# Optimization experiments

Hardware: AMD Instinct MI355X
Metric: run time of the kernel (lower is better)

## Reference

```python
import jax, jax.numpy as jnp
import numpy as np

N_HEADS = 8
N_FILTERS = 512
HEAD_DIM = N_FILTERS // N_HEADS  # key_dim == value_dim == 64
BATCH = 32
SEQ = 4096


def setup_inputs() -> dict:
    key = jax.random.key(0)
    ks = jax.random.split(key, 9)
    s_in = 1.0 / np.sqrt(N_FILTERS)
    s_out = 1.0 / np.sqrt(N_HEADS * HEAD_DIM)
    return {
        "x": jax.random.normal(ks[0], (BATCH, SEQ, N_FILTERS), dtype=jnp.float32),
        # stacked per-head projection weights, stored as [H, in, out]
        "Wq": jax.random.uniform(ks[1], (N_HEADS, N_FILTERS, HEAD_DIM), jnp.float32, -s_in, s_in),
        "bq": jax.random.uniform(ks[2], (N_HEADS, HEAD_DIM), jnp.float32, -s_in, s_in),
        "Wk": jax.random.uniform(ks[3], (N_HEADS, N_FILTERS, HEAD_DIM), jnp.float32, -s_in, s_in),
        "bk": jax.random.uniform(ks[4], (N_HEADS, HEAD_DIM), jnp.float32, -s_in, s_in),
        "Wv": jax.random.uniform(ks[5], (N_HEADS, N_FILTERS, HEAD_DIM), jnp.float32, -s_in, s_in),
        "bv": jax.random.uniform(ks[6], (N_HEADS, HEAD_DIM), jnp.float32, -s_in, s_in),
        "Wo": jax.random.uniform(ks[7], (N_HEADS * HEAD_DIM, N_FILTERS), jnp.float32, -s_out, s_out),
        "bo": jax.random.uniform(ks[8], (N_FILTERS,), jnp.float32, -s_out, s_out),
    }


def reference(x, Wq, bq, Wk, bk, Wv, bv, Wo, bo):
    B, L, F = x.shape
    # Per-head projections, batched over heads: [H, B, L, D]
    Q = jnp.einsum("blf,hfd->hbld", x, Wq) + bq[:, None, None, :]
    K = jnp.einsum("blf,hfd->hbld", x, Wk) + bk[:, None, None, :]
    V = jnp.einsum("blf,hfd->hbld", x, Wv) + bv[:, None, None, :]
    # Feature-space attention: Q^T K -> [H, B, D, D], scale, softmax over dim=1 (rows)
    scores = jnp.einsum("hbld,hble->hbde", Q, K) / np.sqrt(HEAD_DIM).astype(np.float32)
    A = jax.nn.softmax(scores, axis=-2)
    # heads[i] = V @ A : [H, B, L, D]
    heads = jnp.einsum("hbld,hbde->hble", V, A)
    # Faithful to torch: heads.view(batch, l, -1) reinterprets the [H,B,L,D] buffer
    out = heads.reshape(B, L, N_HEADS * HEAD_DIM)
    return out @ Wo + bo
```

## Files before the change

### kernel.cpp

```cpp
#include <hip/hip_runtime.h>
#include <hip/hip_bf16.h>
#include <cstdint>
#include <cstddef>

#define BATCH 32
#define SEQ   4096
#define NF    512
#define NH    8
#define HD    64

typedef __bf16 bf16x8 __attribute__((ext_vector_type(8)));
typedef float  f32x4  __attribute__((ext_vector_type(4)));

__device__ __forceinline__ int lds_off(int m, int kg) {
  return (((m >> 4) * 4 + kg) * 16 + (m & 15)) * 8;
}

template<int MODE>
struct SRegs { bf16x8 h0, h1, l0, l1; };

__device__ __forceinline__ void cvt8(const float* f, bf16x8& vh, bf16x8& vl) {
#pragma unroll
  for (int j = 0; j < 8; ++j) {
    float x = f[j];
    __bf16 h = (__bf16)x;
    vh[j] = h;
    vl[j] = (__bf16)(x - (float)h);
  }
}

template<int MODE>
__device__ __forceinline__ SRegs<MODE> stage_load(
    const void* pa, const void* pb, long long zoff, int ld,
    long long row0, int k0, int tid)
{
  SRegs<MODE> R;
  if constexpr (MODE == 0 || MODE == 3) {
    const __bf16* hi = (const __bf16*)pa + zoff;
    const int r = tid >> 1, half = tid & 1;
    const size_t base = (size_t)(row0 + r) * ld + k0 + half * 16;
    R.h0 = *(const bf16x8*)(hi + base);
    R.h1 = *(const bf16x8*)(hi + base + 8);
    if constexpr (MODE == 0) {
      const __bf16* lo = (const __bf16*)pb + zoff;
      R.l0 = *(const bf16x8*)(lo + base);
      R.l1 = *(const bf16x8*)(lo + base + 8);
    }
  } else if constexpr (MODE == 1) {
    const float* A = (const float*)pa + zoff;
    const int r = tid >> 1, half = tid & 1;
    const float* src = A + (size_t)(row0 + r) * ld + k0 + half * 16;
    float f[16];
#pragma unroll
    for (int q = 0; q < 4; ++q) {
      float4 v = *(const float4*)&src[q * 4];
      f[q * 4 + 0] = v.x; f[q * 4 + 1] = v.y; f[q * 4 + 2] = v.z; f[q * 4 + 3] = v.w;
    }
    cvt8(f, R.h0, R.l0);
    cvt8(f + 8, R.h1, R.l1);
  } else {
    const float* A = (const float*)pa + zoff;
    const int m = tid & 127, lg = (tid >> 7) * 16;
    float f[16];
#pragma unroll
    for (int i = 0; i < 16; ++i)
      f[i] = A[(size_t)(k0 + lg + i) * ld + row0 + m];
    cvt8(f, R.h0, R.l0);
    cvt8(f + 8, R.h1, R.l1);
  }
  return R;
}

template<int MODE>
__device__ __forceinline__ void stage_store(
    const SRegs<MODE>& R, __bf16* sH, __bf16* sL, int tid)
{
  if constexpr (MODE == 2) {
    const int m = tid & 127, kq = (tid >> 7) * 2;
    *(bf16x8*)&sH[lds_off(m, kq + 0)] = R.h0;
    *(bf16x8*)&sH[lds_off(m, kq + 1)] = R.h1;
    *(bf16x8*)&sL[lds_off(m, kq + 0)] = R.l0;
    *(bf16x8*)&sL[lds_off(m, kq + 1)] = R.l1;
  } else {
    const int r = tid >> 1, kq = (tid & 1) * 2;
    *(bf16x8*)&sH[lds_off(r, kq + 0)] = R.h0;
    *(bf16x8*)&sH[lds_off(r, kq + 1)] = R.h1;
    if constexpr (MODE != 3) {
      *(bf16x8*)&sL[lds_off(r, kq + 0)] = R.l0;
      *(bf16x8*)&sL[lds_off(r, kq + 1)] = R.l1;
    }
  }
}

template<int MA, int MB, int EPI>
__global__ __launch_bounds__(256) void mfma_nt(
    const void* Aa, const void* Ab, long long sA, int lda,
    const void* Ba, const void* Bb, long long sB, int ldb,
    const float* __restrict__ bias, void* C0, void* C1, long long sC, int K)
{
  constexpr bool AL = (MA != 3);
  __shared__ __bf16 smem[(AL ? 4 : 3) * 4096];
  __bf16* sAh = smem;
  __bf16* sBh = smem + 4096;
  __bf16* sBl = smem + 8192;
  __bf16* sAl = AL ? (smem + 12288) : smem;

  const int tid = threadIdx.x;
  const int lane = tid & 63, wave = tid >> 6;
  const int wm = wave >> 1, wn = wave & 1;

  const unsigned nx = gridDim.x, ny = gridDim.y;
  const unsigned nwg = nx * ny * gridDim.z;
  unsigned bid = blockIdx.x + nx * (blockIdx.y + ny * blockIdx.z);
  unsigned nid = (bid & 7) * (nwg >> 3) + (bid >> 3);
  const unsigned bx = nid % nx;
  unsigned t = nid / nx;
  const unsigned by = t % ny;
  const unsigned z = t / ny;

  const long long m0 = (long long)by * 128;
  const int n0 = bx * 128;
  const long long zA = (long long)z * sA, zB = (long long)z * sB;

  f32x4 acc[4][4];
#pragma unroll
  for (int i = 0; i < 4; ++i)
#pragma unroll
    for (int j = 0; j < 4; ++j)
#pragma unroll
      for (int c = 0; c < 4; ++c) acc[i][j][c] = 0.f;

  const int kg = lane >> 4, r = lane & 15;

  SRegs<MA> ra = stage_load<MA>(Aa, Ab, zA, lda, m0, 0, tid);
  SRegs<MB> rb = stage_load<MB>(Ba, Bb, zB, ldb, n0, 0, tid);

  for (int k0 = 0; k0 < K; k0 += 32) {
    __syncthreads();
    stage_store<MA>(ra, sAh, sAl, tid);
    stage_store<MB>(rb, sBh, sBl, tid);
    __syncthreads();
    if (k0 + 32 < K) {
      ra = stage_load<MA>(Aa, Ab, zA, lda, m0, k0 + 32, tid);
      rb = stage_load<MB>(Ba, Bb, zB, ldb, n0, k0 + 32, tid);
    }

    bf16x8 ah[4], al[4], bh[4], bl[4];
#pragma unroll
    for (int i = 0; i < 4; ++i) {
      ah[i] = *(const bf16x8*)&sAh[lds_off(wm * 64 + i * 16 + r, kg)];
      if constexpr (AL)
        al[i] = *(const bf16x8*)&sAl[lds_off(wm * 64 + i * 16 + r, kg)];
      bh[i] = *(const bf16x8*)&sBh[lds_off(wn * 64 + i * 16 + r, kg)];
      bl[i] = *(const bf16x8*)&sBl[lds_off(wn * 64 + i * 16 + r, kg)];
    }
#pragma unroll
    for (int i = 0; i < 4; ++i)
#pragma unroll
      for (int j = 0; j < 4; ++j) {
        acc[i][j] = __builtin_amdgcn_mfma_f32_16x16x32_bf16(ah[i], bh[j], acc[i][j], 0, 0, 0);
        if constexpr (AL)
          acc[i][j] = __builtin_amdgcn_mfma_f32_16x16x32_bf16(al[i], bh[j], acc[i][j], 0, 0, 0);
        acc[i][j] = __builtin_amdgcn_mfma_f32_16x16x32_bf16(ah[i], bl[j], acc[i][j], 0, 0, 0);
      }
  }

  const int rbase = (lane >> 4) * 4;
  const int cn = lane & 15;
#pragma unroll
  for (int i = 0; i < 4; ++i) {
    const long long gm = m0 + wm * 64 + i * 16 + rbase;
#pragma unroll
    for (int j = 0; j < 4; ++j) {
      const int gn = n0 + wn * 64 + j * 16 + cn;
      if constexpr (EPI == 0) {
        float* C = (float*)C0 + (long long)z * sC;
#pragma unroll
        for (int rr = 0; rr < 4; ++rr)
          C[(size_t)(gm + rr) * 512 + gn] = acc[i][j][rr];
      } else if constexpr (EPI == 1) {
        float* C = (float*)C0;
        const float bv = bias[gn];
#pragma unroll
        for (int rr = 0; rr < 4; ++rr)
          C[(size_t)(gm + rr) * 512 + gn] = acc[i][j][rr] + bv;
      } else if constexpr (EPI == 2) {
        __bf16* Ch = (__bf16*)C0 + (long long)z * sC;
        __bf16* Cl = (__bf16*)C1 + (long long)z * sC;
#pragma unroll
        for (int rr = 0; rr < 4; ++rr) {
          float v = acc[i][j][rr];
          __bf16 h = (__bf16)v;
          Ch[(size_t)(gm + rr) * 512 + gn] = h;
          Cl[(size_t)(gm + rr) * 512 + gn] = (__bf16)(v - (float)h);
        }
      } else {
        const int h = gn >> 6, e = gn & 63;
        const float bv = bias[(h * 32 + (int)z) * 64 + e];
        __bf16* Ch = (__bf16*)C0;
        const size_t rowb = (size_t)(h * 32 + (int)z) * 4096 + gm;
#pragma unroll
        for (int rr = 0; rr < 4; ++rr)
          Ch[(rowb + rr) * 64 + e] = (__bf16)(acc[i][j][rr] + bv);
      }
    }
  }
}

__global__ void pack3_kernel(const float* __restrict__ Wq, const float* __restrict__ Wk,
                             const float* __restrict__ Wv, const float* __restrict__ Wo,
                             float* __restrict__ Wq_all, float* __restrict__ Wk_all,
                             float* __restrict__ Wv_all,
                             __bf16* __restrict__ Wkt_h, __bf16* __restrict__ Wkt_l,
                             __bf16* __restrict__ Wot_h, __bf16* __restrict__ Wot_l) {
  int i = blockIdx.x * 256 + threadIdx.x;
  if (i >= NF * NF) return;
  int f = i >> 9, n = i & 511, h = n >> 6, d = n & 63;
  size_t src = ((size_t)h * NF + f) * HD + d;
  float wq = Wq[src], wk = Wk[src], wv = Wv[src];
  Wq_all[i] = wq;
  Wk_all[i] = wk;
  Wv_all[i] = wv;
  __bf16 kh = (__bf16)wk;
  Wkt_h[(size_t)n * 512 + f] = kh;
  Wkt_l[(size_t)n * 512 + f] = (__bf16)(wk - (float)kh);
  float wo = Wo[i];
  __bf16 oh = (__bf16)wo;
  Wot_h[(size_t)n * 512 + f] = oh;
  Wot_l[(size_t)n * 512 + f] = (__bf16)(wo - (float)oh);
}

__global__ __launch_bounds__(256) void colsum_kernel(const float* __restrict__ x,
                                                     float* __restrict__ s_part) {
  const int b = blockIdx.x, c = blockIdx.y, t = threadIdx.x;
  const float* base = x + ((size_t)b * SEQ + c * 256) * NF;
  float a0 = 0.f, a1 = 0.f;
  for (int l = 0; l < 256; ++l) {
    a0 += base[(size_t)l * NF + t];
    a1 += base[(size_t)l * NF + t + 256];
  }
  float* o = s_part + ((size_t)b * 16 + c) * NF;
  o[t] = a0;
  o[t + 256] = a1;
}

__global__ __launch_bounds__(256) void pqk_kernel(
    const float* __restrict__ s_part, const float* __restrict__ Wq_all,
    const float* __restrict__ Wk_all, float* __restrict__ pq, float* __restrict__ pk) {
  const int b = blockIdx.x, t = threadIdx.x;
  __shared__ float s[512];
  float a0 = 0.f, a1 = 0.f;
  for (int c = 0; c < 16; ++c) {
    a0 += s_part[((size_t)b * 16 + c) * NF + t];
    a1 += s_part[((size_t)b * 16 + c) * NF + t + 256];
  }
  s[t] = a0;
  s[t + 256] = a1;
  __syncthreads();
  float q0 = 0.f, q1 = 0.f, k0 = 0.f, k1 = 0.f;
  for (int f = 0; f < NF; ++f) {
    const float sv = s[f];
    q0 += sv * Wq_all[(size_t)f * NF + t];
    q1 += sv * Wq_all[(size_t)f * NF + t + 256];
    k0 += sv * Wk_all[(size_t)f * NF + t];
    k1 += sv * Wk_all[(size_t)f * NF + t + 256];
  }
  pq[(size_t)b * NF + t] = q0;
  pq[(size_t)b * NF + t + 256] = q1;
  pk[(size_t)b * NF + t] = k0;
  pk[(size_t)b * NF + t + 256] = k1;
}

__global__ __launch_bounds__(256) void score_softmax_kernel(
    const float* __restrict__ Wq_all, const float* __restrict__ U,
    const float* __restrict__ pq, const float* __restrict__ pk,
    const float* __restrict__ bq, const float* __restrict__ bk,
    const float* __restrict__ bv,
    float* __restrict__ Amat, float* __restrict__ bvA) {
  const int hb = blockIdx.x;
  const int h = hb >> 5, b = hb & 31;
  __shared__ float Qs[64][65];
  __shared__ float Us[64][65];
  __shared__ float Ss[64][65];
  const int tid = threadIdx.x, eg = tid & 15, dg = tid >> 4;
  const float* Ub = U + (size_t)b * NF * NF;

  float acc[4][4];
#pragma unroll
  for (int i = 0; i < 4; ++i)
#pragma unroll
    for (int j = 0; j < 4; ++j) acc[i][j] = 0.f;

  for (int f0 = 0; f0 < NF; f0 += 64) {
#pragma unroll
    for (int q = 0; q < 4; ++q) {
      const int idx = q * 256 + tid;
      const int fi = idx >> 4, dd = (idx & 15) * 4;
      *(float4*)&Qs[fi][dd] = *(const float4*)&Wq_all[(size_t)(f0 + fi) * NF + h * HD + dd];
      *(float4*)&Us[fi][dd] = *(const float4*)&Ub[(size_t)(f0 + fi) * NF + h * HD + dd];
    }
    __syncthreads();
#pragma unroll 16
    for (int fi = 0; fi < 64; ++fi) {
      float4 qa = *(float4*)&Qs[fi][dg * 4];
      float4 ub = *(float4*)&Us[fi][eg * 4];
      float qa_[4] = {qa.x, qa.y, qa.z, qa.w};
      float ub_[4] = {ub.x, ub.y, ub.z, ub.w};
#pragma unroll
      for (int i = 0; i < 4; ++i)
#pragma unroll
        for (int j = 0; j < 4; ++j) acc[i][j] = fmaf(qa_[i], ub_[j], acc[i][j]);
    }
    __syncthreads();
  }

#pragma unroll
  for (int i = 0; i < 4; ++i) {
    const int d = dg * 4 + i;
    const float bqv = bq[h * HD + d];
    const float pqv = pq[(size_t)b * NF + h * HD + d];
#pragma unroll
    for (int j = 0; j < 4; ++j) {
      const int e = eg * 4 + j;
      const float bkv = bk[h * HD + e];
      const float pkv = pk[(size_t)b * NF + h * HD + e];
      float v = acc[i][j] + bqv * pkv + bkv * pqv + 4096.f * bqv * bkv;
      Ss[d][e] = v * 0.125f;
    }
  }
  __syncthreads();

  if (tid < 64) {
    const int e = tid;
    float m = -INFINITY;
    for (int d = 0; d < 64; ++d) m = fmaxf(m, Ss[d][e]);
    float sum = 0.f;
    for (int d = 0; d < 64; ++d) {
      float ex = __expf(Ss[d][e] - m);
      Ss[d][e] = ex;
      sum += ex;
    }
    const float inv = 1.f / sum;
    float bacc = 0.f;
    for (int d = 0; d < 64; ++d) {
      const float a = Ss[d][e] * inv;
      Amat[(size_t)hb * 4096 + d * 64 + e] = a;
      bacc = fmaf(bv[h * HD + d], a, bacc);
    }
    bvA[(size_t)hb * HD + e] = bacc;
  }
}

__global__ __launch_bounds__(256) void wva_kernel(
    const float* __restrict__ Wv_all, const float* __restrict__ Amat,
    __bf16* __restrict__ WvAt_h, __bf16* __restrict__ WvAt_l) {
  const int hb = blockIdx.y, h = hb >> 5, b = hb & 31;
  const int f0 = blockIdx.x * 128;
  __shared__ float Ws[128][65];
  __shared__ float As[64][65];
  const int tid = threadIdx.x;

#pragma unroll
  for (int q = 0; q < 4; ++q) {
    const int idx = q * 256 + tid;
    const int d = idx >> 4, ee = (idx & 15) * 4;
    *(float4*)&As[d][ee] = *(const float4*)&Amat[(size_t)hb * 4096 + d * 64 + ee];
  }
#pragma unroll
  for (int q = 0; q < 8; ++q) {
    const int idx = q * 256 + tid;
    const int fi = idx >> 4, dd = (idx & 15) * 4;
    *(float4*)&Ws[fi][dd] = *(const float4*)&Wv_all[(size_t)(f0 + fi) * NF + h * HD + dd];
  }
  __syncthreads();

  const int fg = tid >> 4, eg = tid & 15;
  float acc[8][4];
#pragma unroll
  for (int i = 0; i < 8; ++i)
#pragma unroll
    for (int j = 0; j < 4; ++j) acc[i][j] = 0.f;
#pragma unroll 8
  for (int d = 0; d < 64; ++d) {
    float4 av = *(float4*)&As[d][eg * 4];
    float a_[4] = {av.x, av.y, av.z, av.w};
#pragma unroll
    for (int i = 0; i < 8; ++i) {
      const float w = Ws[fg * 8 + i][d];
#pragma unroll
      for (int j = 0; j < 4; ++j) acc[i][j] = fmaf(w, a_[j], acc[i][j]);
    }
  }

  __syncthreads();
  float* Ts = &Ws[0][0];
#pragma unroll
  for (int i = 0; i < 8; ++i)
#pragma unroll
    for (int j = 0; j < 4; ++j)
      Ts[(eg * 4 + j) * 130 + fg * 8 + i] = acc[i][j];
  __syncthreads();

  const int e = tid >> 2, fs = (tid & 3) * 32;
  size_t orow = ((size_t)b * 512 + h * 64 + e) * 512 + f0 + fs;
#pragma unroll
  for (int c = 0; c < 4; ++c) {
    bf16x8 vh, vl;
#pragma unroll
    for (int j = 0; j < 8; ++j) {
      float v = Ts[e * 130 + fs + c * 8 + j];
      __bf16 hh = (__bf16)v;
      vh[j] = hh;
      vl[j] = (__bf16)(v - (float)hh);
    }
    *(bf16x8*)&WvAt_h[orow + c * 8] = vh;
    *(bf16x8*)&WvAt_l[orow + c * 8] = vl;
  }
}

extern "C" void kernel_launch(void* const* d_in, const int* in_sizes, int n_in,
                              void* d_out, int out_size, void* d_ws, size_t ws_size,
                              hipStream_t stream) {
  const float* x  = (const float*)d_in[0];
  const float* Wq = (const float*)d_in[1];
  const float* bq = (const float*)d_in[2];
  const float* Wk = (const float*)d_in[3];
  const float* bk = (const float*)d_in[4];
  const float* Wv = (const float*)d_in[5];
  const float* bv = (const float*)d_in[6];
  const float* Wo = (const float*)d_in[7];
  const float* bo = (const float*)d_in[8];
  float* out = (float*)d_out;
  (void)in_sizes; (void)n_in; (void)out_size; (void)ws_size;

  float* w = (float*)d_ws;
  size_t off = 0;
  float* Wq_all = w + off; off += 262144;
  float* Wk_all = w + off; off += 262144;
  float* Wv_all = w + off; off += 262144;
  float* s_part = w + off; off += 262144;
  float* pq     = w + off; off += 16384;
  float* pk     = w + off; off += 16384;
  float* U      = w + off; off += (size_t)32 * 262144;
  float* Amat   = w + off; off += 1048576;
  float* bvA    = w + off; off += 16384;
  __bf16* Wkt_h = (__bf16*)(w + off); off += 131072;
  __bf16* Wkt_l = (__bf16*)(w + off); off += 131072;
  __bf16* Wot_h = (__bf16*)(w + off); off += 131072;
  __bf16* Wot_l = (__bf16*)(w + off); off += 131072;
  __bf16* Gh    = (__bf16*)(w + off); off += (size_t)32 * 131072;
  __bf16* Gl    = (__bf16*)(w + off); off += (size_t)32 * 131072;
  __bf16* WvAt_h= (__bf16*)(w + off); off += (size_t)32 * 131072;
  __bf16* WvAt_l= (__bf16*)(w + off); off += (size_t)32 * 131072;
  __bf16* Hh    = (__bf16*)(w + off); off += (size_t)131072 * 256;

  pack3_kernel<<<1024, 256, 0, stream>>>(Wq, Wk, Wv, Wo, Wq_all, Wk_all, Wv_all,
                                         Wkt_h, Wkt_l, Wot_h, Wot_l);
  colsum_kernel<<<dim3(BATCH, 16), 256, 0, stream>>>(x, s_part);
  pqk_kernel<<<BATCH, 256, 0, stream>>>(s_part, Wq_all, Wk_all, pq, pk);
  mfma_nt<2, 2, 2><<<dim3(4, 4, BATCH), 256, 0, stream>>>(
      x, nullptr, (long long)SEQ * NF, NF,
      x, nullptr, (long long)SEQ * NF, NF,
      nullptr, Gh, Gl, 262144, SEQ);
  mfma_nt<0, 0, 0><<<dim3(4, 4, BATCH), 256, 0, stream>>>(
      Gh, Gl, 262144, NF,
      Wkt_h, Wkt_l, 0, NF,
      nullptr, U, nullptr, 262144, NF);
  score_softmax_kernel<<<256, 256, 0, stream>>>(Wq_all, U, pq, pk, bq, bk, bv,
                                                Amat, bvA);
  wva_kernel<<<dim3(4, 256), 256, 0, stream>>>(Wv_all, Amat, WvAt_h, WvAt_l);
  mfma_nt<1, 0, 3><<<dim3(4, 32, BATCH), 256, 0, stream>>>(
      x, nullptr, (long long)SEQ * NF, NF,
      WvAt_h, WvAt_l, 262144, NF,
      bvA, Hh, nullptr, 0, NF);
  mfma_nt<3, 0, 1><<<dim3(4, 1024, 1), 256, 0, stream>>>(
      Hh, nullptr, 0, NF,
      Wot_h, Wot_l, 0, NF,
      bo, out, nullptr, 0, NF);
}
```

Measured before the change: 1.183 ms.

## Drop bf16 split-precision on V and output GEMMs, exploit Gram symmetry, parallelize softmax

Two GEMMs now run on plain bf16 operands instead of hi/lo splits. That is the x·WvA projection (A from fp32 x, B from WvA) and the heads·Wo output projection. Each loses its correction MFMAs, the low-part LDS traffic and the low-part global writes. The x^T x Gram GEMM now computes only the 10 upper-triangular 128x128 tiles per batch and mirrors off-diagonal tiles with a transposed store. The softmax column reduction now uses all 256 threads with a shared-memory cross-group reduction instead of 64 serial threads. Accuracy drops to single-bf16 for the value and output paths, and the transposed mirror stores are strided.

New measurement: 1.085 ms. 1.09x faster.

```diff
diff --git a/kernel.cpp b/kernel.cpp
--- a/kernel.cpp
+++ b/kernel.cpp
@@ -10,6 +10,7 @@
 #define HD    64
 
 typedef __bf16 bf16x8 __attribute__((ext_vector_type(8)));
+typedef __bf16 bf16x4 __attribute__((ext_vector_type(4)));
 typedef float  f32x4  __attribute__((ext_vector_type(4)));
 
 __device__ __forceinline__ int lds_off(int m, int kg) {
@@ -46,7 +47,7 @@
       R.l0 = *(const bf16x8*)(lo + base);
       R.l1 = *(const bf16x8*)(lo + base + 8);
     }
-  } else if constexpr (MODE == 1) {
+  } else if constexpr (MODE == 1 || MODE == 4) {
     const float* A = (const float*)pa + zoff;
     const int r = tid >> 1, half = tid & 1;
     const float* src = A + (size_t)(row0 + r) * ld + k0 + half * 16;
@@ -56,8 +57,16 @@
       float4 v = *(const float4*)&src[q * 4];
       f[q * 4 + 0] = v.x; f[q * 4 + 1] = v.y; f[q * 4 + 2] = v.z; f[q * 4 + 3] = v.w;
     }
-    cvt8(f, R.h0, R.l0);
-    cvt8(f + 8, R.h1, R.l1);
+    if constexpr (MODE == 1) {
+      cvt8(f, R.h0, R.l0);
+      cvt8(f + 8, R.h1, R.l1);
+    } else {
+#pragma unroll
+      for (int j = 0; j < 8; ++j) {
+        R.h0[j] = (__bf16)f[j];
+        R.h1[j] = (__bf16)f[8 + j];
+      }
+    }
   } else {
     const float* A = (const float*)pa + zoff;
     const int m = tid & 127, lg = (tid >> 7) * 16;
@@ -85,25 +94,27 @@
     const int r = tid >> 1, kq = (tid & 1) * 2;
     *(bf16x8*)&sH[lds_off(r, kq + 0)] = R.h0;
     *(bf16x8*)&sH[lds_off(r, kq + 1)] = R.h1;
-    if constexpr (MODE != 3) {
+    if constexpr (MODE == 0 || MODE == 1) {
       *(bf16x8*)&sL[lds_off(r, kq + 0)] = R.l0;
       *(bf16x8*)&sL[lds_off(r, kq + 1)] = R.l1;
     }
   }
 }
 
-template<int MA, int MB, int EPI>
+template<int MA, int MB, int EPI, bool SYM = false>
 __global__ __launch_bounds__(256) void mfma_nt(
     const void* Aa, const void* Ab, long long sA, int lda,
     const void* Ba, const void* Bb, long long sB, int ldb,
     const float* __restrict__ bias, void* C0, void* C1, long long sC, int K)
 {
-  constexpr bool AL = (MA != 3);
-  __shared__ __bf16 smem[(AL ? 4 : 3) * 4096];
+  constexpr bool AL = (MA <= 2);
+  constexpr bool BL = (MB <= 2);
+  constexpr int NBUF = 2 + (AL ? 1 : 0) + (BL ? 1 : 0);
+  __shared__ __bf16 smem[NBUF * 4096];
   __bf16* sAh = smem;
   __bf16* sBh = smem + 4096;
-  __bf16* sBl = smem + 8192;
-  __bf16* sAl = AL ? (smem + 12288) : smem;
+  __bf16* sAl = AL ? (smem + 8192) : smem;
+  __bf16* sBl = BL ? (smem + (AL ? 12288 : 8192)) : smem;
 
   const int tid = threadIdx.x;
   const int lane = tid & 63, wave = tid >> 6;
@@ -118,8 +129,20 @@
   const unsigned by = t % ny;
   const unsigned z = t / ny;
 
-  const long long m0 = (long long)by * 128;
-  const int n0 = bx * 128;
+  unsigned ti = 0, tj = 0;
+  long long m0;
+  int n0;
+  if constexpr (SYM) {
+    if (bx < 4)      { ti = 0; tj = bx; }
+    else if (bx < 7) { ti = 1; tj = bx - 3; }
+    else if (bx < 9) { ti = 2; tj = bx - 5; }
+    else             { ti = 3; tj = 3; }
+    m0 = (long long)ti * 128;
+    n0 = tj * 128;
+  } else {
+    m0 = (long long)by * 128;
+    n0 = bx * 128;
+  }
   const long long zA = (long long)z * sA, zB = (long long)z * sB;
 
   f32x4 acc[4][4];
@@ -152,7 +175,8 @@
       if constexpr (AL)
         al[i] = *(const bf16x8*)&sAl[lds_off(wm * 64 + i * 16 + r, kg)];
       bh[i] = *(const bf16x8*)&sBh[lds_off(wn * 64 + i * 16 + r, kg)];
-      bl[i] = *(const bf16x8*)&sBl[lds_off(wn * 64 + i * 16 + r, kg)];
+      if constexpr (BL)
+        bl[i] = *(const bf16x8*)&sBl[lds_off(wn * 64 + i * 16 + r, kg)];
     }
 #pragma unroll
     for (int i = 0; i < 4; ++i)
@@ -161,7 +185,8 @@
         acc[i][j] = __builtin_amdgcn_mfma_f32_16x16x32_bf16(ah[i], bh[j], acc[i][j], 0, 0, 0);
         if constexpr (AL)
           acc[i][j] = __builtin_amdgcn_mfma_f32_16x16x32_bf16(al[i], bh[j], acc[i][j], 0, 0, 0);
-        acc[i][j] = __builtin_amdgcn_mfma_f32_16x16x32_bf16(ah[i], bl[j], acc[i][j], 0, 0, 0);
+        if constexpr (BL)
+          acc[i][j] = __builtin_amdgcn_mfma_f32_16x16x32_bf16(ah[i], bl[j], acc[i][j], 0, 0, 0);
       }
   }
 
@@ -187,12 +212,21 @@
       } else if constexpr (EPI == 2) {
         __bf16* Ch = (__bf16*)C0 + (long long)z * sC;
         __bf16* Cl = (__bf16*)C1 + (long long)z * sC;
+        bf16x4 th, tl;
 #pragma unroll
         for (int rr = 0; rr < 4; ++rr) {
           float v = acc[i][j][rr];
           __bf16 h = (__bf16)v;
+          th[rr] = h;
+          tl[rr] = (__bf16)(v - (float)h);
           Ch[(size_t)(gm + rr) * 512 + gn] = h;
-          Cl[(size_t)(gm + rr) * 512 + gn] = (__bf16)(v - (float)h);
+          Cl[(size_t)(gm + rr) * 512 + gn] = tl[rr];
+        }
+        if constexpr (SYM) {
+          if (ti != tj) {
+            *(bf16x4*)&Ch[(size_t)gn * 512 + gm] = th;
+            *(bf16x4*)&Cl[(size_t)gn * 512 + gm] = tl;
+          }
         }
       } else {
         const int h = gn >> 6, e = gn & 63;
@@ -212,7 +246,7 @@
                              float* __restrict__ Wq_all, float* __restrict__ Wk_all,
                              float* __restrict__ Wv_all,
                              __bf16* __restrict__ Wkt_h, __bf16* __restrict__ Wkt_l,
-                             __bf16* __restrict__ Wot_h, __bf16* __restrict__ Wot_l) {
+                             __bf16* __restrict__ Wot_h) {
   int i = blockIdx.x * 256 + threadIdx.x;
   if (i >= NF * NF) return;
   int f = i >> 9, n = i & 511, h = n >> 6, d = n & 63;
@@ -224,10 +258,7 @@
   __bf16 kh = (__bf16)wk;
   Wkt_h[(size_t)n * 512 + f] = kh;
   Wkt_l[(size_t)n * 512 + f] = (__bf16)(wk - (float)kh);
-  float wo = Wo[i];
-  __bf16 oh = (__bf16)wo;
-  Wot_h[(size_t)n * 512 + f] = oh;
-  Wot_l[(size_t)n * 512 + f] = (__bf16)(wo - (float)oh);
+  Wot_h[(size_t)n * 512 + f] = (__bf16)Wo[i];
 }
 
 __global__ __launch_bounds__(256) void colsum_kernel(const float* __restrict__ x,
@@ -282,6 +313,7 @@
   __shared__ float Qs[64][65];
   __shared__ float Us[64][65];
   __shared__ float Ss[64][65];
+  __shared__ float red[4][64];
   const int tid = threadIdx.x, eg = tid & 15, dg = tid >> 4;
   const float* Ub = U + (size_t)b * NF * NF;
 
@@ -330,30 +362,42 @@
   }
   __syncthreads();
 
-  if (tid < 64) {
-    const int e = tid;
-    float m = -INFINITY;
-    for (int d = 0; d < 64; ++d) m = fmaxf(m, Ss[d][e]);
-    float sum = 0.f;
-    for (int d = 0; d < 64; ++d) {
-      float ex = __expf(Ss[d][e] - m);
-      Ss[d][e] = ex;
-      sum += ex;
-    }
-    const float inv = 1.f / sum;
-    float bacc = 0.f;
-    for (int d = 0; d < 64; ++d) {
-      const float a = Ss[d][e] * inv;
-      Amat[(size_t)hb * 4096 + d * 64 + e] = a;
-      bacc = fmaf(bv[h * HD + d], a, bacc);
-    }
-    bvA[(size_t)hb * HD + e] = bacc;
-  }
+  const int e = tid & 63, q = tid >> 6;
+  float pm = -INFINITY;
+#pragma unroll
+  for (int d = 0; d < 16; ++d) pm = fmaxf(pm, Ss[q * 16 + d][e]);
+  red[q][e] = pm;
+  __syncthreads();
+  const float m = fmaxf(fmaxf(red[0][e], red[1][e]), fmaxf(red[2][e], red[3][e]));
+  __syncthreads();
+  float ps = 0.f;
+#pragma unroll
+  for (int d = 0; d < 16; ++d) {
+    float ex = __expf(Ss[q * 16 + d][e] - m);
+    Ss[q * 16 + d][e] = ex;
+    ps += ex;
+  }
+  red[q][e] = ps;
+  __syncthreads();
+  const float inv = 1.f / (red[0][e] + red[1][e] + red[2][e] + red[3][e]);
+  __syncthreads();
+  float bacc = 0.f;
+#pragma unroll
+  for (int d = 0; d < 16; ++d) {
+    const int dd = q * 16 + d;
+    const float a = Ss[dd][e] * inv;
+    Amat[(size_t)hb * 4096 + dd * 64 + e] = a;
+    bacc = fmaf(bv[h * HD + dd], a, bacc);
+  }
+  red[q][e] = bacc;
+  __syncthreads();
+  if (tid < 64)
+    bvA[(size_t)hb * HD + tid] = red[0][tid] + red[1][tid] + red[2][tid] + red[3][tid];
 }
 
 __global__ __launch_bounds__(256) void wva_kernel(
     const float* __restrict__ Wv_all, const float* __restrict__ Amat,
-    __bf16* __restrict__ WvAt_h, __bf16* __restrict__ WvAt_l) {
+    __bf16* __restrict__ WvAt_h) {
   const int hb = blockIdx.y, h = hb >> 5, b = hb & 31;
   const int f0 = blockIdx.x * 128;
   __shared__ float Ws[128][65];
@@ -405,16 +449,11 @@
   size_t orow = ((size_t)b * 512 + h * 64 + e) * 512 + f0 + fs;
 #pragma unroll
   for (int c = 0; c < 4; ++c) {
-    bf16x8 vh, vl;
-#pragma unroll
-    for (int j = 0; j < 8; ++j) {
-      float v = Ts[e * 130 + fs + c * 8 + j];
-      __bf16 hh = (__bf16)v;
-      vh[j] = hh;
-      vl[j] = (__bf16)(v - (float)hh);
-    }
+    bf16x8 vh;
+#pragma unroll
+    for (int j = 0; j < 8; ++j)
+      vh[j] = (__bf16)Ts[e * 130 + fs + c * 8 + j];
     *(bf16x8*)&WvAt_h[orow + c * 8] = vh;
-    *(bf16x8*)&WvAt_l[orow + c * 8] = vl;
   }
 }
 
@@ -447,18 +486,16 @@
   __bf16* Wkt_h = (__bf16*)(w + off); off += 131072;
   __bf16* Wkt_l = (__bf16*)(w + off); off += 131072;
   __bf16* Wot_h = (__bf16*)(w + off); off += 131072;
-  __bf16* Wot_l = (__bf16*)(w + off); off += 131072;
   __bf16* Gh    = (__bf16*)(w + off); off += (size_t)32 * 131072;
   __bf16* Gl    = (__bf16*)(w + off); off += (size_t)32 * 131072;
   __bf16* WvAt_h= (__bf16*)(w + off); off += (size_t)32 * 131072;
-  __bf16* WvAt_l= (__bf16*)(w + off); off += (size_t)32 * 131072;
   __bf16* Hh    = (__bf16*)(w + off); off += (size_t)131072 * 256;
 
   pack3_kernel<<<1024, 256, 0, stream>>>(Wq, Wk, Wv, Wo, Wq_all, Wk_all, Wv_all,
-                                         Wkt_h, Wkt_l, Wot_h, Wot_l);
+                                         Wkt_h, Wkt_l, Wot_h);
   colsum_kernel<<<dim3(BATCH, 16), 256, 0, stream>>>(x, s_part);
   pqk_kernel<<<BATCH, 256, 0, stream>>>(s_part, Wq_all, Wk_all, pq, pk);
-  mfma_nt<2, 2, 2><<<dim3(4, 4, BATCH), 256, 0, stream>>>(
+  mfma_nt<2, 2, 2, true><<<dim3(10, 1, BATCH), 256, 0, stream>>>(
       x, nullptr, (long long)SEQ * NF, NF,
       x, nullptr, (long long)SEQ * NF, NF,
       nullptr, Gh, Gl, 262144, SEQ);
@@ -468,13 +505,13 @@
       nullptr, U, nullptr, 262144, NF);
   score_softmax_kernel<<<256, 256, 0, stream>>>(Wq_all, U, pq, pk, bq, bk, bv,
                                                 Amat, bvA);
-  wva_kernel<<<dim3(4, 256), 256, 0, stream>>>(Wv_all, Amat, WvAt_h, WvAt_l);
-  mfma_nt<1, 0, 3><<<dim3(4, 32, BATCH), 256, 0, stream>>>(
+  wva_kernel<<<dim3(4, 256), 256, 0, stream>>>(Wv_all, Amat, WvAt_h);
+  mfma_nt<4, 3, 3><<<dim3(4, 32, BATCH), 256, 0, stream>>>(
       x, nullptr, (long long)SEQ * NF, NF,
-      WvAt_h, WvAt_l, 262144, NF,
+      WvAt_h, nullptr, 262144, NF,
       bvA, Hh, nullptr, 0, NF);
-  mfma_nt<3, 0, 1><<<dim3(4, 1024, 1), 256, 0, stream>>>(
+  mfma_nt<3, 3, 1><<<dim3(4, 1024, 1), 256, 0, stream>>>(
       Hh, nullptr, 0, NF,
-      Wot_h, Wot_l, 0, NF,
+      Wot_h, nullptr, 0, NF,
       bo, out, nullptr, 0, NF);
 }
```
